# Performance work log

Hardware: AMD Instinct MI355X
Metric: run time of the kernel (lower is better)

The kernel has to match this reference:

```python
import jax, jax.numpy as jnp
import numpy as np

B, S, I, H, A = 512, 256, 12, 256, 9


def _lstm_layer(x, w_ih, w_hh, b_ih, b_hh):
    # x: [B,S,in] -> outputs [B,S,H], final (h, c). PyTorch gate order i,f,g,o.
    b, s, _ = x.shape
    h_dim = w_hh.shape[1]
    xg = jnp.einsum('bsi,gi->bsg', x, w_ih) + b_ih  # [B,S,4H] precomputed input gates

    def step(carry, xg_t):
        h, c = carry
        gates = xg_t + h @ w_hh.T + b_hh
        i_g, f_g, g_g, o_g = jnp.split(gates, 4, axis=-1)
        c = jax.nn.sigmoid(f_g) * c + jax.nn.sigmoid(i_g) * jnp.tanh(g_g)
        h = jax.nn.sigmoid(o_g) * jnp.tanh(c)
        return (h, c), h

    init = (jnp.zeros((b, h_dim), x.dtype), jnp.zeros((b, h_dim), x.dtype))
    (h, c), ys = jax.lax.scan(step, init, jnp.swapaxes(xg, 0, 1))
    return jnp.swapaxes(ys, 0, 1), h, c


def setup_inputs() -> dict:
    key = jax.random.key(0)
    ks = jax.random.split(key, 20)
    sc = 0.1
    inp = {
        'x': jax.random.normal(ks[0], (B, S, I), jnp.float32),
        'mask': jnp.ones((B, A), jnp.float32),
        'W_emb': jax.random.normal(ks[1], (H, I), jnp.float32) * sc,
        'b_emb': jnp.zeros((H,), jnp.float32),
        'w_ih0': jax.random.normal(ks[2], (4 * H, H), jnp.float32) * sc,
        'w_hh0': jax.random.normal(ks[3], (4 * H, H), jnp.float32) * sc,
        'b_ih0': jnp.zeros((4 * H,), jnp.float32),
        'b_hh0': jnp.zeros((4 * H,), jnp.float32),
        'w_ih1': jax.random.normal(ks[4], (4 * H, H), jnp.float32) * sc,
        'w_hh1': jax.random.normal(ks[5], (4 * H, H), jnp.float32) * sc,
        'b_ih1': jnp.zeros((4 * H,), jnp.float32),
        'b_hh1': jnp.zeros((4 * H,), jnp.float32),
        'ln_g': jnp.ones((H,), jnp.float32),
        'ln_b': jnp.zeros((H,), jnp.float32),
        'w1': jax.random.normal(ks[6], (32, H), jnp.float32) * sc,
        'b1': jnp.zeros((32,), jnp.float32),
        'w2': jax.random.normal(ks[7], (A, 32), jnp.float32) * sc,
        'b2': jnp.zeros((A,), jnp.float32),
    }
    return inp


def reference(x, mask, W_emb, b_emb, w_ih0, w_hh0, b_ih0, b_hh0,
              w_ih1, w_hh1, b_ih1, b_hh1, ln_g, ln_b, w1, b1, w2, b2):
    # embed + ReLU
    emb = jax.nn.relu(jnp.einsum('bsi,hi->bsh', x, W_emb) + b_emb)  # [B,S,H]
    # 2-layer LSTM (dropout between layers is identity in eval mode)
    y0, h0, c0 = _lstm_layer(emb, w_ih0, w_hh0, b_ih0, b_hh0)
    y1, h1, c1 = _lstm_layer(y0, w_ih1, w_hh1, b_ih1, b_hh1)
    last = y1[:, -1, :]  # [B,H]
    # LayerNorm
    mu = jnp.mean(last, axis=-1, keepdims=True)
    var = jnp.mean((last - mu) ** 2, axis=-1, keepdims=True)
    normed = (last - mu) / jnp.sqrt(var + 1e-5) * ln_g + ln_b
    # MLP head (dropout identity in eval)
    hdn = jax.nn.relu(normed @ w1.T + b1)
    logits = hdn @ w2.T + b2  # [B,A]
    logits = logits + (1.0 - mask) * -1e9
    hidden = (jnp.stack([h0, h1]), jnp.stack([c0, c1]))
    return logits, hidden
```

## Files before the change

kernel.cpp:

```cpp
#include <hip/hip_runtime.h>
#include <cstdint>
#include <cstddef>

typedef __attribute__((ext_vector_type(8))) short short8;
typedef __attribute__((ext_vector_type(4))) float f32x4;

#define MFMA16(a, b, c) __builtin_amdgcn_mfma_f32_16x16x32_bf16((a), (b), (c), 0, 0, 0)

constexpr int kB = 512, kS = 256, kI = 12, kH = 256, kA = 9;
constexpr int kNS = 8;
constexpr int kNB = 32;
constexpr int kT  = 512;
constexpr int LDH = 264;
constexpr int LDG = 132;
constexpr int kBH = kB * kH;
constexpr int FLS = 512;

constexpr int OUT_H = kB * kA;
constexpr int OUT_C = OUT_H + 2 * kBH;

__device__ __forceinline__ short f2bf(float f) {
  uint32_t u = __float_as_uint(f);
  u += 0x7fffu + ((u >> 16) & 1u);
  return (short)(u >> 16);
}
__device__ __forceinline__ float fast_sigmoid(float v) {
  return __builtin_amdgcn_rcpf(1.f + __expf(-v));
}
__device__ __forceinline__ float fast_tanh(float v) {
  return 2.f * __builtin_amdgcn_rcpf(1.f + __expf(-2.f * v)) - 1.f;
}

__global__ __launch_bounds__(kT, 2) void lstm_scan_kernel(
    const float* __restrict__ x,
    const float* __restrict__ W_emb, const float* __restrict__ b_emb,
    const float* __restrict__ w_ih0, const float* __restrict__ w_hh0,
    const float* __restrict__ b_ih0, const float* __restrict__ b_hh0,
    const float* __restrict__ w_ih1, const float* __restrict__ w_hh1,
    const float* __restrict__ b_ih1, const float* __restrict__ b_hh1,
    unsigned short* __restrict__ h0ex, unsigned short* __restrict__ h1ex,
    int* __restrict__ flags,
    float* __restrict__ dout)
{
  const int tid   = threadIdx.x;
  const int btile = blockIdx.x & (kNB - 1);
  const int slice = blockIdx.x >> 5;
  const int b0    = btile * 16;
  const int lane  = tid & 63;
  const int wave  = tid >> 6;
  const int n16   = lane & 15;
  const int quad  = lane >> 4;

  __shared__ short embL[16 * LDH];
  __shared__ short hA[16 * LDH];
  __shared__ short hB[16 * LDH];
  __shared__ float gL0[16 * LDG];
  __shared__ float gL1[16 * LDG];

  for (int i = tid; i < 16 * LDH; i += kT) { hA[i] = 0; hB[i] = 0; }

  const float* Wm[4] = { w_ih0, w_hh0, w_ih1, w_hh1 };
  short8 wB[4][8];
  {
    const int gcol = (wave >> 1) * kH + slice * 32 + (wave & 1) * 16 + n16;
#pragma unroll
    for (int mat = 0; mat < 4; ++mat) {
      const float* wp = Wm[mat] + (size_t)gcol * kH;
#pragma unroll
      for (int kk = 0; kk < 8; ++kk) {
        const float* p = wp + kk * 32 + quad * 8;
        const float4 f0 = *(const float4*)p;
        const float4 f1 = *(const float4*)(p + 4);
        short8 v;
        v[0] = f2bf(f0.x); v[1] = f2bf(f0.y); v[2] = f2bf(f0.z); v[3] = f2bf(f0.w);
        v[4] = f2bf(f1.x); v[5] = f2bf(f1.y); v[6] = f2bf(f1.z); v[7] = f2bf(f1.w);
        wB[mat][kk] = v;
      }
    }
  }
  short8 wE[2];
  float bembv[2];
#pragma unroll
  for (int i = 0; i < 2; ++i) {
    const int col = wave * 32 + i * 16 + n16;
    short8 v;
#pragma unroll
    for (int j = 0; j < 8; ++j) {
      const int k = quad * 8 + j;
      v[j] = (k < kI) ? f2bf(W_emb[col * kI + k]) : (short)0;
    }
    wE[i] = v;
    bembv[i] = b_emb[col];
  }
  const int erow = tid >> 5;
  const int ec   = tid & 31;
  const int ecol = slice * 32 + ec;
  float bi0[4], bi1[4];
#pragma unroll
  for (int g = 0; g < 4; ++g) {
    bi0[g] = b_ih0[g * kH + ecol] + b_hh0[g * kH + ecol];
    bi1[g] = b_ih1[g * kH + ecol] + b_hh1[g * kH + ecol];
  }
  float c0v = 0.f, c1v = 0.f;

  {
    const float* xr = x + (size_t)(b0 + n16) * kS * kI;
    short8 xa;
#pragma unroll
    for (int j = 0; j < 8; ++j) {
      const int k = quad * 8 + j;
      xa[j] = (k < kI) ? f2bf(xr[k]) : (short)0;
    }
#pragma unroll
    for (int i = 0; i < 2; ++i) {
      f32x4 z = {0.f, 0.f, 0.f, 0.f};
      f32x4 e = MFMA16(xa, wE[i], z);
      const int col = wave * 32 + i * 16 + n16;
#pragma unroll
      for (int r = 0; r < 4; ++r) {
        float v = e[r] + bembv[i];
        v = v > 0.f ? v : 0.f;
        embL[(quad * 4 + r) * LDH + col] = f2bf(v);
      }
    }
  }
  __syncthreads();

  int* const fl = flags + btile * FLS;

  for (int p = 0; p <= kS; ++p) {
    const int par = p & 1;

    {
      f32x4 a0 = {0.f,0.f,0.f,0.f}, g1 = a0;
#pragma unroll
      for (int kk = 0; kk < 8; ++kk) {
        const short8 ha = *(const short8*)&hA[n16 * LDH + kk * 32 + quad * 8];
        a0 = MFMA16(ha, wB[1][kk], a0);
        g1 = MFMA16(ha, wB[2][kk], g1);
      }
#pragma unroll
      for (int kk = 0; kk < 8; ++kk) {
        const short8 e = *(const short8*)&embL[n16 * LDH + kk * 32 + quad * 8];
        a0 = MFMA16(e, wB[0][kk], a0);
      }
#pragma unroll
      for (int kk = 0; kk < 8; ++kk) {
        const short8 hb = *(const short8*)&hB[n16 * LDH + kk * 32 + quad * 8];
        g1 = MFMA16(hb, wB[3][kk], g1);
      }
      const int lcol = (wave >> 1) * 32 + (wave & 1) * 16 + n16;
#pragma unroll
      for (int r = 0; r < 4; ++r) {
        gL0[(quad * 4 + r) * LDG + lcol] = a0[r];
        gL1[(quad * 4 + r) * LDG + lcol] = g1[r];
      }
    }
    __syncthreads();

    if (p < kS) {
      const float iv = gL0[erow * LDG +       ec] + bi0[0];
      const float fv = gL0[erow * LDG +  32 + ec] + bi0[1];
      const float gv = gL0[erow * LDG +  64 + ec] + bi0[2];
      const float ov = gL0[erow * LDG +  96 + ec] + bi0[3];
      const float c = fast_sigmoid(fv) * c0v + fast_sigmoid(iv) * fast_tanh(gv);
      c0v = c;
      const float h = fast_sigmoid(ov) * fast_tanh(c);
      unsigned short* dst = &h0ex[(size_t)par * kBH + (size_t)(b0 + erow) * kH + ecol];
      __hip_atomic_store(dst, (unsigned short)f2bf(h), __ATOMIC_RELAXED, __HIP_MEMORY_SCOPE_AGENT);
      if (p == kS - 1) {
        dout[OUT_H + (size_t)(b0 + erow) * kH + ecol] = h;
        dout[OUT_C + (size_t)(b0 + erow) * kH + ecol] = c;
      }
    }
    if (p >= 1) {
      const float iv = gL1[erow * LDG +       ec] + bi1[0];
      const float fv = gL1[erow * LDG +  32 + ec] + bi1[1];
      const float gv = gL1[erow * LDG +  64 + ec] + bi1[2];
      const float ov = gL1[erow * LDG +  96 + ec] + bi1[3];
      const float c = fast_sigmoid(fv) * c1v + fast_sigmoid(iv) * fast_tanh(gv);
      c1v = c;
      const float h = fast_sigmoid(ov) * fast_tanh(c);
      unsigned short* dst = &h1ex[(size_t)par * kBH + (size_t)(b0 + erow) * kH + ecol];
      __hip_atomic_store(dst, (unsigned short)f2bf(h), __ATOMIC_RELAXED, __HIP_MEMORY_SCOPE_AGENT);
      if (p == kS) {
        dout[OUT_H + kBH + (size_t)(b0 + erow) * kH + ecol] = h;
        dout[OUT_C + kBH + (size_t)(b0 + erow) * kH + ecol] = c;
      }
    }
    __syncthreads();

    if (p < kS) {
      if (tid == 0)
        __hip_atomic_fetch_add(fl + p, 1, __ATOMIC_RELAXED, __HIP_MEMORY_SCOPE_AGENT);

      if (p + 1 < kS) {
        const float* xr = x + ((size_t)(b0 + n16) * kS + (p + 1)) * kI;
        short8 xa;
#pragma unroll
        for (int j = 0; j < 8; ++j) {
          const int k = quad * 8 + j;
          xa[j] = (k < kI) ? f2bf(xr[k]) : (short)0;
        }
#pragma unroll
        for (int i = 0; i < 2; ++i) {
          f32x4 z = {0.f, 0.f, 0.f, 0.f};
          f32x4 e = MFMA16(xa, wE[i], z);
          const int col = wave * 32 + i * 16 + n16;
#pragma unroll
          for (int r = 0; r < 4; ++r) {
            float v = e[r] + bembv[i];
            v = v > 0.f ? v : 0.f;
            embL[(quad * 4 + r) * LDH + col] = f2bf(v);
          }
        }
      }

      while (__hip_atomic_load(fl + p, __ATOMIC_RELAXED, __HIP_MEMORY_SCOPE_AGENT) < kNS)
        __builtin_amdgcn_s_sleep(1);

      {
        const int rr = tid >> 5;
        const int cc = (tid & 31) * 8;
        const size_t base = (size_t)par * kBH + (size_t)(b0 + rr) * kH + cc;
        const uint64_t* s0 = (const uint64_t*)&h0ex[base];
        const uint64_t* s1 = (const uint64_t*)&h1ex[base];
        uint64_t va0 = __hip_atomic_load(s0 + 0, __ATOMIC_RELAXED, __HIP_MEMORY_SCOPE_AGENT);
        uint64_t va1 = __hip_atomic_load(s0 + 1, __ATOMIC_RELAXED, __HIP_MEMORY_SCOPE_AGENT);
        uint64_t vb0 = __hip_atomic_load(s1 + 0, __ATOMIC_RELAXED, __HIP_MEMORY_SCOPE_AGENT);
        uint64_t vb1 = __hip_atomic_load(s1 + 1, __ATOMIC_RELAXED, __HIP_MEMORY_SCOPE_AGENT);
        uint64_t* dA = (uint64_t*)&hA[rr * LDH + cc];
        uint64_t* dB = (uint64_t*)&hB[rr * LDH + cc];
        dA[0] = va0; dA[1] = va1;
        dB[0] = vb0; dB[1] = vb1;
      }
      __syncthreads();
    }
  }
}

__global__ __launch_bounds__(64) void head_kernel(
    const float* __restrict__ h1last, const float* __restrict__ mask,
    const float* __restrict__ ln_g, const float* __restrict__ ln_b,
    const float* __restrict__ w1, const float* __restrict__ b1,
    const float* __restrict__ w2, const float* __restrict__ b2,
    float* __restrict__ out)
{
  const int r = blockIdx.x;
  const int lane = threadIdx.x;
  __shared__ float ns[kH];
  __shared__ float hd[32];
  const float4 v = *(const float4*)&h1last[r * kH + lane * 4];
  float vv[4] = {v.x, v.y, v.z, v.w};
  float s = vv[0] + vv[1] + vv[2] + vv[3];
#pragma unroll
  for (int off = 32; off > 0; off >>= 1) s += __shfl_xor(s, off, 64);
  const float mean = s * (1.f / kH);
  float q = 0.f;
#pragma unroll
  for (int j = 0; j < 4; ++j) { const float d = vv[j] - mean; q += d * d; }
#pragma unroll
  for (int off = 32; off > 0; off >>= 1) q += __shfl_xor(q, off, 64);
  const float rstd = rsqrtf(q * (1.f / kH) + 1e-5f);
#pragma unroll
  for (int j = 0; j < 4; ++j) {
    const int c = lane * 4 + j;
    ns[c] = (vv[j] - mean) * rstd * ln_g[c] + ln_b[c];
  }
  __syncthreads();
  if (lane < 32) {
    float a = b1[lane];
    const float* wr = w1 + lane * kH;
    for (int k = 0; k < kH; ++k) a += ns[k] * wr[k];
    hd[lane] = a > 0.f ? a : 0.f;
  }
  __syncthreads();
  if (lane < kA) {
    float a = b2[lane];
    const float* wr = w2 + lane * 32;
#pragma unroll
    for (int k = 0; k < 32; ++k) a += hd[k] * wr[k];
    a += (1.f - mask[r * kA + lane]) * (-1e9f);
    out[r * kA + lane] = a;
  }
}

extern "C" void kernel_launch(void* const* d_in, const int* in_sizes, int n_in,
                              void* d_out, int out_size, void* d_ws, size_t ws_size,
                              hipStream_t stream)
{
  (void)in_sizes; (void)n_in; (void)out_size; (void)ws_size;
  const float* x     = (const float*)d_in[0];
  const float* mask  = (const float*)d_in[1];
  const float* W_emb = (const float*)d_in[2];
  const float* b_emb = (const float*)d_in[3];
  const float* w_ih0 = (const float*)d_in[4];
  const float* w_hh0 = (const float*)d_in[5];
  const float* b_ih0 = (const float*)d_in[6];
  const float* b_hh0 = (const float*)d_in[7];
  const float* w_ih1 = (const float*)d_in[8];
  const float* w_hh1 = (const float*)d_in[9];
  const float* b_ih1 = (const float*)d_in[10];
  const float* b_hh1 = (const float*)d_in[11];
  const float* ln_g  = (const float*)d_in[12];
  const float* ln_b  = (const float*)d_in[13];
  const float* w1    = (const float*)d_in[14];
  const float* b1    = (const float*)d_in[15];
  const float* w2    = (const float*)d_in[16];
  const float* b2    = (const float*)d_in[17];
  float* out = (float*)d_out;

  unsigned short* h0ex = (unsigned short*)d_ws;
  unsigned short* h1ex = h0ex + 2 * kBH;
  int* flags = (int*)(h1ex + 2 * kBH);
  const size_t flag_bytes = (size_t)kNB * FLS * sizeof(int);

  hipMemsetAsync(flags, 0, flag_bytes, stream);
  hipMemsetAsync(h1ex, 0, (size_t)kBH * sizeof(unsigned short), stream);

  lstm_scan_kernel<<<dim3(kNB * kNS), dim3(kT), 0, stream>>>(
      x, W_emb, b_emb, w_ih0, w_hh0, b_ih0, b_hh0, w_ih1, w_hh1, b_ih1, b_hh1,
      h0ex, h1ex, flags, out);

  head_kernel<<<dim3(kB), dim3(64), 0, stream>>>(
      out + OUT_H + kBH, mask, ln_g, ln_b, w1, b1, w2, b2, out);
}
```

Baseline: 1.011 ms.

## Interleave two batch tiles per block to hide cross-block flag wait latency

Each block now processes two 16-row batch tiles (X and Y), alternating them within each timestep. The grid is halved so each block handles both tiles. The spin-wait and gather for one tile is intended to overlap with the other tile's MFMA and elementwise work, hiding the global flag synchronisation latency of the recurrence. In exchange, each block does twice the serial work per step on half as many blocks, adds more __syncthreads per step, and reuses the hA/hB buffers across the two tiles.

```diff
diff --git a/kernel.cpp b/kernel.cpp
--- a/kernel.cpp
+++ b/kernel.cpp
@@ -10,6 +10,7 @@
 constexpr int kB = 512, kS = 256, kI = 12, kH = 256, kA = 9;
 constexpr int kNS = 8;
 constexpr int kNB = 32;
+constexpr int kNP = 16;
 constexpr int kT  = 512;
 constexpr int LDH = 264;
 constexpr int LDG = 132;
@@ -30,6 +31,117 @@
 __device__ __forceinline__ float fast_tanh(float v) {
   return 2.f * __builtin_amdgcn_rcpf(1.f + __expf(-2.f * v)) - 1.f;
 }
+
+
+#define EMB_TILE(EMBA, B0, T)                                               \
+  {                                                                         \
+    const float* xr = x + ((size_t)((B0) + n16) * kS + (T)) * kI;           \
+    short8 xa;                                                              \
+    _Pragma("unroll")                                                       \
+    for (int j = 0; j < 8; ++j) {                                           \
+      const int k = quad * 8 + j;                                           \
+      xa[j] = (k < kI) ? f2bf(xr[k]) : (short)0;                            \
+    }                                                                       \
+    _Pragma("unroll")                                                       \
+    for (int i = 0; i < 2; ++i) {                                           \
+      f32x4 z = {0.f, 0.f, 0.f, 0.f};                                       \
+      f32x4 e = MFMA16(xa, wE[i], z);                                       \
+      const int col = wave * 32 + i * 16 + n16;                             \
+      _Pragma("unroll")                                                     \
+      for (int r = 0; r < 4; ++r) {                                         \
+        float v = e[r] + bembv[i];                                          \
+        v = v > 0.f ? v : 0.f;                                              \
+        EMBA[(quad * 4 + r) * LDH + col] = f2bf(v);                         \
+      }                                                                     \
+    }                                                                       \
+  }
+
+#define HEAD_TILE(EMBA)                                                     \
+  {                                                                         \
+    f32x4 a0 = {0.f, 0.f, 0.f, 0.f}, g1 = a0;                               \
+    _Pragma("unroll")                                                       \
+    for (int kk = 0; kk < 8; ++kk) {                                        \
+      const short8 ha = *(const short8*)&hA[n16 * LDH + kk * 32 + quad * 8];\
+      a0 = MFMA16(ha, wB[1][kk], a0);                                       \
+      g1 = MFMA16(ha, wB[2][kk], g1);                                       \
+    }                                                                       \
+    _Pragma("unroll")                                                       \
+    for (int kk = 0; kk < 8; ++kk) {                                        \
+      const short8 e = *(const short8*)&EMBA[n16 * LDH + kk * 32 + quad*8]; \
+      a0 = MFMA16(e, wB[0][kk], a0);                                        \
+    }                                                                       \
+    _Pragma("unroll")                                                       \
+    for (int kk = 0; kk < 8; ++kk) {                                        \
+      const short8 hb = *(const short8*)&hB[n16 * LDH + kk * 32 + quad*8];  \
+      g1 = MFMA16(hb, wB[3][kk], g1);                                       \
+    }                                                                       \
+    const int lcol = (wave >> 1) * 32 + (wave & 1) * 16 + n16;              \
+    _Pragma("unroll")                                                       \
+    for (int r = 0; r < 4; ++r) {                                           \
+      gL0[(quad * 4 + r) * LDG + lcol] = a0[r];                             \
+      gL1[(quad * 4 + r) * LDG + lcol] = g1[r];                             \
+    }                                                                       \
+  }
+
+#define ELEM_L0(B0, C0V)                                                    \
+  if (p < kS) {                                                             \
+    const float iv = gL0[erow * LDG +       ec] + bi0[0];                   \
+    const float fv = gL0[erow * LDG +  32 + ec] + bi0[1];                   \
+    const float gv = gL0[erow * LDG +  64 + ec] + bi0[2];                   \
+    const float ov = gL0[erow * LDG +  96 + ec] + bi0[3];                   \
+    const float c = fast_sigmoid(fv) * (C0V) + fast_sigmoid(iv) * fast_tanh(gv); \
+    (C0V) = c;                                                              \
+    const float h = fast_sigmoid(ov) * fast_tanh(c);                        \
+    unsigned short* dst =                                                   \
+        &h0ex[(size_t)par * kBH + (size_t)((B0) + erow) * kH + ecol];       \
+    __hip_atomic_store(dst, (unsigned short)f2bf(h), __ATOMIC_RELAXED,      \
+                       __HIP_MEMORY_SCOPE_AGENT);                           \
+    if (p == kS - 1) {                                                      \
+      dout[OUT_H + (size_t)((B0) + erow) * kH + ecol] = h;                  \
+      dout[OUT_C + (size_t)((B0) + erow) * kH + ecol] = c;                  \
+    }                                                                       \
+  }
+
+#define ELEM_L1(B0, C1V)                                                    \
+  if (p >= 1) {                                                             \
+    const float iv = gL1[erow * LDG +       ec] + bi1[0];                   \
+    const float fv = gL1[erow * LDG +  32 + ec] + bi1[1];                   \
+    const float gv = gL1[erow * LDG +  64 + ec] + bi1[2];                   \
+    const float ov = gL1[erow * LDG +  96 + ec] + bi1[3];                   \
+    const float c = fast_sigmoid(fv) * (C1V) + fast_sigmoid(iv) * fast_tanh(gv); \
+    (C1V) = c;                                                              \
+    const float h = fast_sigmoid(ov) * fast_tanh(c);                        \
+    unsigned short* dst =                                                   \
+        &h1ex[(size_t)par * kBH + (size_t)((B0) + erow) * kH + ecol];       \
+    __hip_atomic_store(dst, (unsigned short)f2bf(h), __ATOMIC_RELAXED,      \
+                       __HIP_MEMORY_SCOPE_AGENT);                           \
+    if (p == kS) {                                                          \
+      dout[OUT_H + kBH + (size_t)((B0) + erow) * kH + ecol] = h;            \
+      dout[OUT_C + kBH + (size_t)((B0) + erow) * kH + ecol] = c;            \
+    }                                                                       \
+  }
+
+#define GATHER_TILE(B0)                                                     \
+  {                                                                         \
+    const int rr = tid >> 5;                                                \
+    const int cc = (tid & 31) * 8;                                          \
+    const size_t base = (size_t)parg * kBH + (size_t)((B0) + rr) * kH + cc; \
+    const uint64_t* s0 = (const uint64_t*)&h0ex[base];                      \
+    const uint64_t* s1 = (const uint64_t*)&h1ex[base];                      \
+    uint64_t va0 = __hip_atomic_load(s0 + 0, __ATOMIC_RELAXED, __HIP_MEMORY_SCOPE_AGENT); \
+    uint64_t va1 = __hip_atomic_load(s0 + 1, __ATOMIC_RELAXED, __HIP_MEMORY_SCOPE_AGENT); \
+    uint64_t vb0 = __hip_atomic_load(s1 + 0, __ATOMIC_RELAXED, __HIP_MEMORY_SCOPE_AGENT); \
+    uint64_t vb1 = __hip_atomic_load(s1 + 1, __ATOMIC_RELAXED, __HIP_MEMORY_SCOPE_AGENT); \
+    uint64_t* dA = (uint64_t*)&hA[rr * LDH + cc];                           \
+    uint64_t* dB = (uint64_t*)&hB[rr * LDH + cc];                           \
+    dA[0] = va0; dA[1] = va1;                                               \
+    dB[0] = vb0; dB[1] = vb1;                                               \
+  }
+
+#define SPIN_WAIT(FL)                                                       \
+  while (__hip_atomic_load((FL) + (p - 1), __ATOMIC_RELAXED,                \
+                           __HIP_MEMORY_SCOPE_AGENT) < kNS)                 \
+    __builtin_amdgcn_s_sleep(1);
 
 __global__ __launch_bounds__(kT, 2) void lstm_scan_kernel(
     const float* __restrict__ x,
@@ -43,15 +155,17 @@
     float* __restrict__ dout)
 {
   const int tid   = threadIdx.x;
-  const int btile = blockIdx.x & (kNB - 1);
-  const int slice = blockIdx.x >> 5;
-  const int b0    = btile * 16;
+  const int pair  = blockIdx.x & (kNP - 1);
+  const int slice = blockIdx.x >> 4;
+  const int b0X   = pair * 16;
+  const int b0Y   = (pair + 16) * 16;
   const int lane  = tid & 63;
   const int wave  = tid >> 6;
   const int n16   = lane & 15;
   const int quad  = lane >> 4;
 
-  __shared__ short embL[16 * LDH];
+  __shared__ short embX[16 * LDH];
+  __shared__ short embY[16 * LDH];
   __shared__ short hA[16 * LDH];
   __shared__ short hB[16 * LDH];
   __shared__ float gL0[16 * LDG];
@@ -101,140 +215,42 @@
     bi0[g] = b_ih0[g * kH + ecol] + b_hh0[g * kH + ecol];
     bi1[g] = b_ih1[g * kH + ecol] + b_hh1[g * kH + ecol];
   }
-  float c0v = 0.f, c1v = 0.f;
-
-  {
-    const float* xr = x + (size_t)(b0 + n16) * kS * kI;
-    short8 xa;
-#pragma unroll
-    for (int j = 0; j < 8; ++j) {
-      const int k = quad * 8 + j;
-      xa[j] = (k < kI) ? f2bf(xr[k]) : (short)0;
-    }
-#pragma unroll
-    for (int i = 0; i < 2; ++i) {
-      f32x4 z = {0.f, 0.f, 0.f, 0.f};
-      f32x4 e = MFMA16(xa, wE[i], z);
-      const int col = wave * 32 + i * 16 + n16;
-#pragma unroll
-      for (int r = 0; r < 4; ++r) {
-        float v = e[r] + bembv[i];
-        v = v > 0.f ? v : 0.f;
-        embL[(quad * 4 + r) * LDH + col] = f2bf(v);
-      }
-    }
-  }
+  float c0X = 0.f, c1X = 0.f, c0Y = 0.f, c1Y = 0.f;
+
+  EMB_TILE(embX, b0X, 0);
+  EMB_TILE(embY, b0Y, 0);
   __syncthreads();
 
-  int* const fl = flags + btile * FLS;
+  int* const flX = flags + pair * FLS;
+  int* const flY = flags + (pair + 16) * FLS;
 
   for (int p = 0; p <= kS; ++p) {
-    const int par = p & 1;
-
-    {
-      f32x4 a0 = {0.f,0.f,0.f,0.f}, g1 = a0;
-#pragma unroll
-      for (int kk = 0; kk < 8; ++kk) {
-        const short8 ha = *(const short8*)&hA[n16 * LDH + kk * 32 + quad * 8];
-        a0 = MFMA16(ha, wB[1][kk], a0);
-        g1 = MFMA16(ha, wB[2][kk], g1);
-      }
-#pragma unroll
-      for (int kk = 0; kk < 8; ++kk) {
-        const short8 e = *(const short8*)&embL[n16 * LDH + kk * 32 + quad * 8];
-        a0 = MFMA16(e, wB[0][kk], a0);
-      }
-#pragma unroll
-      for (int kk = 0; kk < 8; ++kk) {
-        const short8 hb = *(const short8*)&hB[n16 * LDH + kk * 32 + quad * 8];
-        g1 = MFMA16(hb, wB[3][kk], g1);
-      }
-      const int lcol = (wave >> 1) * 32 + (wave & 1) * 16 + n16;
-#pragma unroll
-      for (int r = 0; r < 4; ++r) {
-        gL0[(quad * 4 + r) * LDG + lcol] = a0[r];
-        gL1[(quad * 4 + r) * LDG + lcol] = g1[r];
-      }
-    }
-    __syncthreads();
-
-    if (p < kS) {
-      const float iv = gL0[erow * LDG +       ec] + bi0[0];
-      const float fv = gL0[erow * LDG +  32 + ec] + bi0[1];
-      const float gv = gL0[erow * LDG +  64 + ec] + bi0[2];
-      const float ov = gL0[erow * LDG +  96 + ec] + bi0[3];
-      const float c = fast_sigmoid(fv) * c0v + fast_sigmoid(iv) * fast_tanh(gv);
-      c0v = c;
-      const float h = fast_sigmoid(ov) * fast_tanh(c);
-      unsigned short* dst = &h0ex[(size_t)par * kBH + (size_t)(b0 + erow) * kH + ecol];
-      __hip_atomic_store(dst, (unsigned short)f2bf(h), __ATOMIC_RELAXED, __HIP_MEMORY_SCOPE_AGENT);
-      if (p == kS - 1) {
-        dout[OUT_H + (size_t)(b0 + erow) * kH + ecol] = h;
-        dout[OUT_C + (size_t)(b0 + erow) * kH + ecol] = c;
-      }
-    }
-    if (p >= 1) {
-      const float iv = gL1[erow * LDG +       ec] + bi1[0];
-      const float fv = gL1[erow * LDG +  32 + ec] + bi1[1];
-      const float gv = gL1[erow * LDG +  64 + ec] + bi1[2];
-      const float ov = gL1[erow * LDG +  96 + ec] + bi1[3];
-      const float c = fast_sigmoid(fv) * c1v + fast_sigmoid(iv) * fast_tanh(gv);
-      c1v = c;
-      const float h = fast_sigmoid(ov) * fast_tanh(c);
-      unsigned short* dst = &h1ex[(size_t)par * kBH + (size_t)(b0 + erow) * kH + ecol];
-      __hip_atomic_store(dst, (unsigned short)f2bf(h), __ATOMIC_RELAXED, __HIP_MEMORY_SCOPE_AGENT);
-      if (p == kS) {
-        dout[OUT_H + kBH + (size_t)(b0 + erow) * kH + ecol] = h;
-        dout[OUT_C + kBH + (size_t)(b0 + erow) * kH + ecol] = c;
-      }
-    }
-    __syncthreads();
-
-    if (p < kS) {
-      if (tid == 0)
-        __hip_atomic_fetch_add(fl + p, 1, __ATOMIC_RELAXED, __HIP_MEMORY_SCOPE_AGENT);
-
-      if (p + 1 < kS) {
-        const float* xr = x + ((size_t)(b0 + n16) * kS + (p + 1)) * kI;
-        short8 xa;
-#pragma unroll
-        for (int j = 0; j < 8; ++j) {
-          const int k = quad * 8 + j;
-          xa[j] = (k < kI) ? f2bf(xr[k]) : (short)0;
-        }
-#pragma unroll
-        for (int i = 0; i < 2; ++i) {
-          f32x4 z = {0.f, 0.f, 0.f, 0.f};
-          f32x4 e = MFMA16(xa, wE[i], z);
-          const int col = wave * 32 + i * 16 + n16;
-#pragma unroll
-          for (int r = 0; r < 4; ++r) {
-            float v = e[r] + bembv[i];
-            v = v > 0.f ? v : 0.f;
-            embL[(quad * 4 + r) * LDH + col] = f2bf(v);
-          }
-        }
-      }
-
-      while (__hip_atomic_load(fl + p, __ATOMIC_RELAXED, __HIP_MEMORY_SCOPE_AGENT) < kNS)
-        __builtin_amdgcn_s_sleep(1);
-
-      {
-        const int rr = tid >> 5;
-        const int cc = (tid & 31) * 8;
-        const size_t base = (size_t)par * kBH + (size_t)(b0 + rr) * kH + cc;
-        const uint64_t* s0 = (const uint64_t*)&h0ex[base];
-        const uint64_t* s1 = (const uint64_t*)&h1ex[base];
-        uint64_t va0 = __hip_atomic_load(s0 + 0, __ATOMIC_RELAXED, __HIP_MEMORY_SCOPE_AGENT);
-        uint64_t va1 = __hip_atomic_load(s0 + 1, __ATOMIC_RELAXED, __HIP_MEMORY_SCOPE_AGENT);
-        uint64_t vb0 = __hip_atomic_load(s1 + 0, __ATOMIC_RELAXED, __HIP_MEMORY_SCOPE_AGENT);
-        uint64_t vb1 = __hip_atomic_load(s1 + 1, __ATOMIC_RELAXED, __HIP_MEMORY_SCOPE_AGENT);
-        uint64_t* dA = (uint64_t*)&hA[rr * LDH + cc];
-        uint64_t* dB = (uint64_t*)&hB[rr * LDH + cc];
-        dA[0] = va0; dA[1] = va1;
-        dB[0] = vb0; dB[1] = vb1;
-      }
-      __syncthreads();
+    const int par  = p & 1;
+    const int parg = par ^ 1;
+
+    if (p >= 1) { SPIN_WAIT(flX); GATHER_TILE(b0X); }
+    __syncthreads();
+    HEAD_TILE(embX);
+    __syncthreads();
+    ELEM_L0(b0X, c0X);
+    ELEM_L1(b0X, c1X);
+    __syncthreads();
+    if (p < kS && tid == 0)
+      __hip_atomic_fetch_add(flX + p, 1, __ATOMIC_RELAXED, __HIP_MEMORY_SCOPE_AGENT);
+
+    if (p >= 1) { SPIN_WAIT(flY); GATHER_TILE(b0Y); }
+    __syncthreads();
+    HEAD_TILE(embY);
+    __syncthreads();
+    ELEM_L0(b0Y, c0Y);
+    ELEM_L1(b0Y, c1Y);
+    __syncthreads();
+    if (p < kS && tid == 0)
+      __hip_atomic_fetch_add(flY + p, 1, __ATOMIC_RELAXED, __HIP_MEMORY_SCOPE_AGENT);
+
+    if (p + 1 < kS) {
+      EMB_TILE(embX, b0X, p + 1);
+      EMB_TILE(embY, b0Y, p + 1);
     }
   }
 }
@@ -318,7 +334,7 @@
   hipMemsetAsync(flags, 0, flag_bytes, stream);
   hipMemsetAsync(h1ex, 0, (size_t)kBH * sizeof(unsigned short), stream);
 
-  lstm_scan_kernel<<<dim3(kNB * kNS), dim3(kT), 0, stream>>>(
+  lstm_scan_kernel<<<dim3(kNP * kNS), dim3(kT), 0, stream>>>(
       x, W_emb, b_emb, w_ih0, w_hh0, b_ih0, b_hh0, w_ih1, w_hh1, b_ih1, b_hh1,
       h0ex, h1ex, flags, out);
 
```

New measurement: 1.828 ms. 1.81x slower.

## Split hidden slices across 16 blocks with split-K partial gate sums

Applied to the files above, without the earlier changes.

Each batch tile is now spread over 16 slices of 16 hidden columns instead of 8 slices of 32, with 256-thread blocks. Each wave computes half of the K dimension, so partial gate sums are written to shared memory and added during the elementwise step. The wait-and-fetch of the previous hidden state moves to the start of each step, so the embedding computation for the next step overlaps the wait. This spreads the serial recurrence over more blocks, which cuts per-block MFMA work but doubles the number of blocks each flag barrier must wait for, adding synchronisation cost.

```diff
diff --git a/kernel.cpp b/kernel.cpp
--- a/kernel.cpp
+++ b/kernel.cpp
@@ -8,11 +8,11 @@
 #define MFMA16(a, b, c) __builtin_amdgcn_mfma_f32_16x16x32_bf16((a), (b), (c), 0, 0, 0)
 
 constexpr int kB = 512, kS = 256, kI = 12, kH = 256, kA = 9;
-constexpr int kNS = 8;
+constexpr int kNS = 16;
 constexpr int kNB = 32;
-constexpr int kT  = 512;
+constexpr int kT  = 256;
 constexpr int LDH = 264;
-constexpr int LDG = 132;
+constexpr int LDG2 = 66;
 constexpr int kBH = kB * kH;
 constexpr int FLS = 512;
 
@@ -30,6 +30,7 @@
 __device__ __forceinline__ float fast_tanh(float v) {
   return 2.f * __builtin_amdgcn_rcpf(1.f + __expf(-2.f * v)) - 1.f;
 }
+
 
 __global__ __launch_bounds__(kT, 2) void lstm_scan_kernel(
     const float* __restrict__ x,
@@ -50,39 +51,43 @@
   const int wave  = tid >> 6;
   const int n16   = lane & 15;
   const int quad  = lane >> 4;
+  const int kh    = wave >> 1;
+  const int cg    = wave & 1;
 
   __shared__ short embL[16 * LDH];
   __shared__ short hA[16 * LDH];
   __shared__ short hB[16 * LDH];
-  __shared__ float gL0[16 * LDG];
-  __shared__ float gL1[16 * LDG];
+  __shared__ float gP[2][2][16 * LDG2];
 
   for (int i = tid; i < 16 * LDH; i += kT) { hA[i] = 0; hB[i] = 0; }
 
   const float* Wm[4] = { w_ih0, w_hh0, w_ih1, w_hh1 };
-  short8 wB[4][8];
+  short8 wB[4][2][4];
   {
-    const int gcol = (wave >> 1) * kH + slice * 32 + (wave & 1) * 16 + n16;
 #pragma unroll
     for (int mat = 0; mat < 4; ++mat) {
-      const float* wp = Wm[mat] + (size_t)gcol * kH;
-#pragma unroll
-      for (int kk = 0; kk < 8; ++kk) {
-        const float* p = wp + kk * 32 + quad * 8;
-        const float4 f0 = *(const float4*)p;
-        const float4 f1 = *(const float4*)(p + 4);
-        short8 v;
-        v[0] = f2bf(f0.x); v[1] = f2bf(f0.y); v[2] = f2bf(f0.z); v[3] = f2bf(f0.w);
-        v[4] = f2bf(f1.x); v[5] = f2bf(f1.y); v[6] = f2bf(f1.z); v[7] = f2bf(f1.w);
-        wB[mat][kk] = v;
-      }
-    }
-  }
-  short8 wE[2];
-  float bembv[2];
-#pragma unroll
-  for (int i = 0; i < 2; ++i) {
-    const int col = wave * 32 + i * 16 + n16;
+#pragma unroll
+      for (int f = 0; f < 2; ++f) {
+        const int gcol = (cg * 2 + f) * kH + slice * 16 + n16;
+        const float* wp = Wm[mat] + (size_t)gcol * kH + kh * 128;
+#pragma unroll
+        for (int kkk = 0; kkk < 4; ++kkk) {
+          const float* p = wp + kkk * 32 + quad * 8;
+          const float4 f0 = *(const float4*)p;
+          const float4 f1 = *(const float4*)(p + 4);
+          short8 v;
+          v[0] = f2bf(f0.x); v[1] = f2bf(f0.y); v[2] = f2bf(f0.z); v[3] = f2bf(f0.w);
+          v[4] = f2bf(f1.x); v[5] = f2bf(f1.y); v[6] = f2bf(f1.z); v[7] = f2bf(f1.w);
+          wB[mat][f][kkk] = v;
+        }
+      }
+    }
+  }
+  short8 wE[4];
+  float bembv[4];
+#pragma unroll
+  for (int i = 0; i < 4; ++i) {
+    const int col = wave * 64 + i * 16 + n16;
     short8 v;
 #pragma unroll
     for (int j = 0; j < 8; ++j) {
@@ -92,9 +97,9 @@
     wE[i] = v;
     bembv[i] = b_emb[col];
   }
-  const int erow = tid >> 5;
-  const int ec   = tid & 31;
-  const int ecol = slice * 32 + ec;
+  const int erow = tid >> 4;
+  const int ec   = tid & 15;
+  const int ecol = slice * 16 + ec;
   float bi0[4], bi1[4];
 #pragma unroll
   for (int g = 0; g < 4; ++g) {
@@ -103,66 +108,102 @@
   }
   float c0v = 0.f, c1v = 0.f;
 
-  {
-    const float* xr = x + (size_t)(b0 + n16) * kS * kI;
-    short8 xa;
-#pragma unroll
-    for (int j = 0; j < 8; ++j) {
-      const int k = quad * 8 + j;
-      xa[j] = (k < kI) ? f2bf(xr[k]) : (short)0;
-    }
-#pragma unroll
-    for (int i = 0; i < 2; ++i) {
-      f32x4 z = {0.f, 0.f, 0.f, 0.f};
-      f32x4 e = MFMA16(xa, wE[i], z);
-      const int col = wave * 32 + i * 16 + n16;
-#pragma unroll
-      for (int r = 0; r < 4; ++r) {
-        float v = e[r] + bembv[i];
-        v = v > 0.f ? v : 0.f;
-        embL[(quad * 4 + r) * LDH + col] = f2bf(v);
-      }
-    }
-  }
+#define EMB_TILE(T)                                                         \
+  {                                                                         \
+    const float* xr = x + ((size_t)(b0 + n16) * kS + (T)) * kI;             \
+    short8 xa;                                                              \
+    _Pragma("unroll")                                                       \
+    for (int j = 0; j < 8; ++j) {                                           \
+      const int k = quad * 8 + j;                                           \
+      xa[j] = (k < kI) ? f2bf(xr[k]) : (short)0;                            \
+    }                                                                       \
+    _Pragma("unroll")                                                       \
+    for (int i = 0; i < 4; ++i) {                                           \
+      f32x4 z = {0.f, 0.f, 0.f, 0.f};                                       \
+      f32x4 e = MFMA16(xa, wE[i], z);                                       \
+      const int col = wave * 64 + i * 16 + n16;                             \
+      _Pragma("unroll")                                                     \
+      for (int r = 0; r < 4; ++r) {                                         \
+        float v = e[r] + bembv[i];                                          \
+        v = v > 0.f ? v : 0.f;                                              \
+        embL[(quad * 4 + r) * LDH + col] = f2bf(v);                         \
+      }                                                                     \
+    }                                                                       \
+  }
+
+  EMB_TILE(0);
   __syncthreads();
 
   int* const fl = flags + btile * FLS;
 
   for (int p = 0; p <= kS; ++p) {
-    const int par = p & 1;
+    const int par  = p & 1;
+    const int parg = par ^ 1;
+
+    if (p >= 1) {
+      while (__hip_atomic_load(fl + (p - 1), __ATOMIC_RELAXED,
+                               __HIP_MEMORY_SCOPE_AGENT) < kNS)
+        __builtin_amdgcn_s_sleep(1);
+      const int rr = tid >> 4;
+      const int cc = (tid & 15) * 16;
+      const size_t base = (size_t)parg * kBH + (size_t)(b0 + rr) * kH + cc;
+      const uint64_t* s0 = (const uint64_t*)&h0ex[base];
+      const uint64_t* s1 = (const uint64_t*)&h1ex[base];
+      uint64_t a0 = __hip_atomic_load(s0 + 0, __ATOMIC_RELAXED, __HIP_MEMORY_SCOPE_AGENT);
+      uint64_t a1 = __hip_atomic_load(s0 + 1, __ATOMIC_RELAXED, __HIP_MEMORY_SCOPE_AGENT);
+      uint64_t a2 = __hip_atomic_load(s0 + 2, __ATOMIC_RELAXED, __HIP_MEMORY_SCOPE_AGENT);
+      uint64_t a3 = __hip_atomic_load(s0 + 3, __ATOMIC_RELAXED, __HIP_MEMORY_SCOPE_AGENT);
+      uint64_t b0_ = __hip_atomic_load(s1 + 0, __ATOMIC_RELAXED, __HIP_MEMORY_SCOPE_AGENT);
+      uint64_t b1_ = __hip_atomic_load(s1 + 1, __ATOMIC_RELAXED, __HIP_MEMORY_SCOPE_AGENT);
+      uint64_t b2_ = __hip_atomic_load(s1 + 2, __ATOMIC_RELAXED, __HIP_MEMORY_SCOPE_AGENT);
+      uint64_t b3_ = __hip_atomic_load(s1 + 3, __ATOMIC_RELAXED, __HIP_MEMORY_SCOPE_AGENT);
+      uint64_t* dA = (uint64_t*)&hA[rr * LDH + cc];
+      uint64_t* dB = (uint64_t*)&hB[rr * LDH + cc];
+      dA[0] = a0; dA[1] = a1; dA[2] = a2; dA[3] = a3;
+      dB[0] = b0_; dB[1] = b1_; dB[2] = b2_; dB[3] = b3_;
+    }
+    __syncthreads();
 
     {
-      f32x4 a0 = {0.f,0.f,0.f,0.f}, g1 = a0;
-#pragma unroll
-      for (int kk = 0; kk < 8; ++kk) {
-        const short8 ha = *(const short8*)&hA[n16 * LDH + kk * 32 + quad * 8];
-        a0 = MFMA16(ha, wB[1][kk], a0);
-        g1 = MFMA16(ha, wB[2][kk], g1);
-      }
-#pragma unroll
-      for (int kk = 0; kk < 8; ++kk) {
-        const short8 e = *(const short8*)&embL[n16 * LDH + kk * 32 + quad * 8];
-        a0 = MFMA16(e, wB[0][kk], a0);
-      }
-#pragma unroll
-      for (int kk = 0; kk < 8; ++kk) {
-        const short8 hb = *(const short8*)&hB[n16 * LDH + kk * 32 + quad * 8];
-        g1 = MFMA16(hb, wB[3][kk], g1);
-      }
-      const int lcol = (wave >> 1) * 32 + (wave & 1) * 16 + n16;
-#pragma unroll
-      for (int r = 0; r < 4; ++r) {
-        gL0[(quad * 4 + r) * LDG + lcol] = a0[r];
-        gL1[(quad * 4 + r) * LDG + lcol] = g1[r];
+      f32x4 a0[2] = {{0.f,0.f,0.f,0.f},{0.f,0.f,0.f,0.f}};
+      f32x4 g1[2] = {{0.f,0.f,0.f,0.f},{0.f,0.f,0.f,0.f}};
+#pragma unroll
+      for (int kkk = 0; kkk < 4; ++kkk) {
+        const short8 ha = *(const short8*)&hA[n16 * LDH + (kh * 4 + kkk) * 32 + quad * 8];
+        a0[0] = MFMA16(ha, wB[1][0][kkk], a0[0]);
+        a0[1] = MFMA16(ha, wB[1][1][kkk], a0[1]);
+        g1[0] = MFMA16(ha, wB[2][0][kkk], g1[0]);
+        g1[1] = MFMA16(ha, wB[2][1][kkk], g1[1]);
+      }
+#pragma unroll
+      for (int kkk = 0; kkk < 4; ++kkk) {
+        const short8 e = *(const short8*)&embL[n16 * LDH + (kh * 4 + kkk) * 32 + quad * 8];
+        a0[0] = MFMA16(e, wB[0][0][kkk], a0[0]);
+        a0[1] = MFMA16(e, wB[0][1][kkk], a0[1]);
+      }
+#pragma unroll
+      for (int kkk = 0; kkk < 4; ++kkk) {
+        const short8 hb = *(const short8*)&hB[n16 * LDH + (kh * 4 + kkk) * 32 + quad * 8];
+        g1[0] = MFMA16(hb, wB[3][0][kkk], g1[0]);
+        g1[1] = MFMA16(hb, wB[3][1][kkk], g1[1]);
+      }
+#pragma unroll
+      for (int f = 0; f < 2; ++f) {
+        const int lcol = cg * 32 + f * 16 + n16;
+#pragma unroll
+        for (int r = 0; r < 4; ++r) {
+          gP[kh][0][(quad * 4 + r) * LDG2 + lcol] = a0[f][r];
+          gP[kh][1][(quad * 4 + r) * LDG2 + lcol] = g1[f][r];
+        }
       }
     }
     __syncthreads();
 
     if (p < kS) {
-      const float iv = gL0[erow * LDG +       ec] + bi0[0];
-      const float fv = gL0[erow * LDG +  32 + ec] + bi0[1];
-      const float gv = gL0[erow * LDG +  64 + ec] + bi0[2];
-      const float ov = gL0[erow * LDG +  96 + ec] + bi0[3];
+      const float iv = gP[0][0][erow * LDG2 +      ec] + gP[1][0][erow * LDG2 +      ec] + bi0[0];
+      const float fv = gP[0][0][erow * LDG2 + 16 + ec] + gP[1][0][erow * LDG2 + 16 + ec] + bi0[1];
+      const float gv = gP[0][0][erow * LDG2 + 32 + ec] + gP[1][0][erow * LDG2 + 32 + ec] + bi0[2];
+      const float ov = gP[0][0][erow * LDG2 + 48 + ec] + gP[1][0][erow * LDG2 + 48 + ec] + bi0[3];
       const float c = fast_sigmoid(fv) * c0v + fast_sigmoid(iv) * fast_tanh(gv);
       c0v = c;
       const float h = fast_sigmoid(ov) * fast_tanh(c);
@@ -174,10 +215,10 @@
       }
     }
     if (p >= 1) {
-      const float iv = gL1[erow * LDG +       ec] + bi1[0];
-      const float fv = gL1[erow * LDG +  32 + ec] + bi1[1];
-      const float gv = gL1[erow * LDG +  64 + ec] + bi1[2];
-      const float ov = gL1[erow * LDG +  96 + ec] + bi1[3];
+      const float iv = gP[0][1][erow * LDG2 +      ec] + gP[1][1][erow * LDG2 +      ec] + bi1[0];
+      const float fv = gP[0][1][erow * LDG2 + 16 + ec] + gP[1][1][erow * LDG2 + 16 + ec] + bi1[1];
+      const float gv = gP[0][1][erow * LDG2 + 32 + ec] + gP[1][1][erow * LDG2 + 32 + ec] + bi1[2];
+      const float ov = gP[0][1][erow * LDG2 + 48 + ec] + gP[1][1][erow * LDG2 + 48 + ec] + bi1[3];
       const float c = fast_sigmoid(fv) * c1v + fast_sigmoid(iv) * fast_tanh(gv);
       c1v = c;
       const float h = fast_sigmoid(ov) * fast_tanh(c);
@@ -194,49 +235,10 @@
       if (tid == 0)
         __hip_atomic_fetch_add(fl + p, 1, __ATOMIC_RELAXED, __HIP_MEMORY_SCOPE_AGENT);
 
-      if (p + 1 < kS) {
-        const float* xr = x + ((size_t)(b0 + n16) * kS + (p + 1)) * kI;
-        short8 xa;
-#pragma unroll
-        for (int j = 0; j < 8; ++j) {
-          const int k = quad * 8 + j;
-          xa[j] = (k < kI) ? f2bf(xr[k]) : (short)0;
-        }
-#pragma unroll
-        for (int i = 0; i < 2; ++i) {
-          f32x4 z = {0.f, 0.f, 0.f, 0.f};
-          f32x4 e = MFMA16(xa, wE[i], z);
-          const int col = wave * 32 + i * 16 + n16;
-#pragma unroll
-          for (int r = 0; r < 4; ++r) {
-            float v = e[r] + bembv[i];
-            v = v > 0.f ? v : 0.f;
-            embL[(quad * 4 + r) * LDH + col] = f2bf(v);
-          }
-        }
-      }
-
-      while (__hip_atomic_load(fl + p, __ATOMIC_RELAXED, __HIP_MEMORY_SCOPE_AGENT) < kNS)
-        __builtin_amdgcn_s_sleep(1);
-
-      {
-        const int rr = tid >> 5;
-        const int cc = (tid & 31) * 8;
-        const size_t base = (size_t)par * kBH + (size_t)(b0 + rr) * kH + cc;
-        const uint64_t* s0 = (const uint64_t*)&h0ex[base];
-        const uint64_t* s1 = (const uint64_t*)&h1ex[base];
-        uint64_t va0 = __hip_atomic_load(s0 + 0, __ATOMIC_RELAXED, __HIP_MEMORY_SCOPE_AGENT);
-        uint64_t va1 = __hip_atomic_load(s0 + 1, __ATOMIC_RELAXED, __HIP_MEMORY_SCOPE_AGENT);
-        uint64_t vb0 = __hip_atomic_load(s1 + 0, __ATOMIC_RELAXED, __HIP_MEMORY_SCOPE_AGENT);
-        uint64_t vb1 = __hip_atomic_load(s1 + 1, __ATOMIC_RELAXED, __HIP_MEMORY_SCOPE_AGENT);
-        uint64_t* dA = (uint64_t*)&hA[rr * LDH + cc];
-        uint64_t* dB = (uint64_t*)&hB[rr * LDH + cc];
-        dA[0] = va0; dA[1] = va1;
-        dB[0] = vb0; dB[1] = vb1;
-      }
-      __syncthreads();
-    }
-  }
+      if (p + 1 < kS) EMB_TILE(p + 1);
+    }
+  }
+#undef EMB_TILE
 }
 
 __global__ __launch_bounds__(64) void head_kernel(
```

Result: slower. 1.493 ms (+47.7%).
